# Kernel optimization log

Measured on AMD Instinct MI355X. Metric: run time of the kernel, lower is better.

Reference implementation:

```python
import jax, jax.numpy as jnp
import numpy as np

I_DIM, H_DIM, O_DIM = 4, 8, 1


def setup_inputs() -> dict:
    key = jax.random.key(0)
    ks = jax.random.split(key, 7)
    B, T = 8192, 512
    s_ih = 1.0 / np.sqrt(H_DIM)
    x = jax.random.normal(ks[0], (B, T, I_DIM), dtype=jnp.float32)
    # PyTorch LSTM params: gate order i, f, g, o stacked along first axis (4H)
    W_ih = jax.random.uniform(ks[1], (4 * H_DIM, I_DIM), jnp.float32, -s_ih, s_ih)
    W_hh = jax.random.uniform(ks[2], (4 * H_DIM, H_DIM), jnp.float32, -s_ih, s_ih)
    b_ih = jax.random.uniform(ks[3], (4 * H_DIM,), jnp.float32, -s_ih, s_ih)
    b_hh = jax.random.uniform(ks[4], (4 * H_DIM,), jnp.float32, -s_ih, s_ih)
    W_fc = jax.random.uniform(ks[5], (O_DIM, H_DIM), jnp.float32, -s_ih, s_ih)
    b_fc = jax.random.uniform(ks[6], (O_DIM,), jnp.float32, -s_ih, s_ih)
    return {"x": x, "W_ih": W_ih, "W_hh": W_hh, "b_ih": b_ih, "b_hh": b_hh,
            "W_fc": W_fc, "b_fc": b_fc}


def _lstm_last_hidden(x, W_ih, W_hh, b_ih, b_hh):
    B, T, _ = x.shape
    H = W_hh.shape[1]
    # Precompute input projections for all timesteps: [B, T, 4H] -> [T, B, 4H]
    xg = jnp.einsum('bti,gi->btg', x, W_ih) + b_ih + b_hh
    xg = jnp.transpose(xg, (1, 0, 2))
    h0 = jnp.zeros((B, H), x.dtype)
    c0 = jnp.zeros((B, H), x.dtype)

    def step(carry, g_t):
        h, c = carry
        gates = g_t + h @ W_hh.T  # [B, 4H]
        i, f, g, o = jnp.split(gates, 4, axis=-1)
        i = jax.nn.sigmoid(i)
        f = jax.nn.sigmoid(f)
        g = jnp.tanh(g)
        o = jax.nn.sigmoid(o)
        c = f * c + i * g
        h = o * jnp.tanh(c)
        return (h, c), None

    (h_last, _), _ = jax.lax.scan(step, (h0, c0), xg)
    return h_last  # equals out[:, -1, :]


def reference(x, W_ih, W_hh, b_ih, b_hh, W_fc, b_fc):
    h_last = _lstm_last_hidden(x, W_ih, W_hh, b_ih, b_hh)
    return h_last @ W_fc.T + b_fc  # [B, output_dim]
```

## Files before the change

kernel.cpp:

```cpp
#include <hip/hip_runtime.h>

#define T_STEPS 512
#define CHUNK   32
#define NCHUNK  (T_STEPS / CHUNK)
#define EPB     32
#define ROWF    132
#define BUFF    (EPB * ROWF)
#define LOG2E   1.4426950408889634f

typedef float v2f __attribute__((ext_vector_type(2)));

__device__ __forceinline__ v2f pk_fma_b(v2f w, float s, v2f c) {
    v2f sv; sv.x = s;
    v2f d;
    asm("v_pk_fma_f32 %0, %1, %2, %3 op_sel_hi:[1,0,1]"
        : "=v"(d) : "v"(w), "v"(sv), "v"(c));
    return d;
}
__device__ __forceinline__ void pk_fma_acc(v2f& a, v2f w, float s) {
    v2f sv; sv.x = s;
    asm("v_pk_fma_f32 %0, %1, %2, %0 op_sel_hi:[1,0,1]"
        : "+v"(a) : "v"(w), "v"(sv));
}
__device__ __forceinline__ v2f pk_mul_b(v2f w, float s) {
    v2f sv; sv.x = s;
    v2f d;
    asm("v_pk_mul_f32 %0, %1, %2 op_sel_hi:[1,0]"
        : "=v"(d) : "v"(w), "v"(sv));
    return d;
}
__device__ __forceinline__ v2f pk_add2(v2f a, v2f b) {
    v2f d;
    asm("v_pk_add_f32 %0, %1, %2" : "=v"(d) : "v"(a), "v"(b));
    return d;
}

template <int CTRL>
__device__ __forceinline__ float dppf(float v) {
    return __int_as_float(__builtin_amdgcn_update_dpp(
        0, __float_as_int(v), CTRL, 0xF, 0xF, true));
}

__global__ __launch_bounds__(256) void lstm_kernel(
    const float* __restrict__ x, const float* __restrict__ W_ih,
    const float* __restrict__ W_hh, const float* __restrict__ b_ih,
    const float* __restrict__ b_hh, const float* __restrict__ W_fc,
    const float* __restrict__ b_fc, float* __restrict__ out, int B)
{
    __shared__ float ldsx[2 * BUFF];

    const int tid = threadIdx.x;
    const int e   = tid >> 3;
    const int j   = tid & 7;

    const float nL  = -LOG2E;
    const float n2L = -2.0f * LOG2E;
    const float P2L =  2.0f * LOG2E;

    const int ri = j, rf = 8 + j, rg = 16 + j, ro = 24 + j;
    v2f wihIF[4], wihGO[4], whhIF[8], whhGO[8], biasIF, biasGO;
    #pragma unroll
    for (int k = 0; k < 4; ++k) {
        wihIF[k] = v2f{nL  * W_ih[ri * 4 + k], nL * W_ih[rf * 4 + k]};
        wihGO[k] = v2f{n2L * W_ih[rg * 4 + k], nL * W_ih[ro * 4 + k]};
    }
    #pragma unroll
    for (int s = 0; s < 8; ++s) {
        const int m = j ^ s;
        whhIF[s] = v2f{nL  * W_hh[ri * 8 + m], nL * W_hh[rf * 8 + m]};
        whhGO[s] = v2f{n2L * W_hh[rg * 8 + m], nL * W_hh[ro * 8 + m]};
    }
    biasIF = v2f{nL  * (b_ih[ri] + b_hh[ri]), nL * (b_ih[rf] + b_hh[rf])};
    biasGO = v2f{n2L * (b_ih[rg] + b_hh[rg]), nL * (b_ih[ro] + b_hh[ro])};

    const int st  = tid & 31;
    const int se0 = tid >> 5;
    const float* gp0 = x + (size_t)(blockIdx.x * EPB + se0) * (T_STEPS * 4) + st * 4;
    const int wl0 = se0 * ROWF + st * 4;

    float4 v0, v1, v2, v3;
    v0 = *(const float4*)(gp0);
    v1 = *(const float4*)(gp0 + 8 * 2048);
    v2 = *(const float4*)(gp0 + 16 * 2048);
    v3 = *(const float4*)(gp0 + 24 * 2048);
    *(float4*)&ldsx[wl0 + 0 * 8 * ROWF] = v0;
    *(float4*)&ldsx[wl0 + 1 * 8 * ROWF] = v1;
    *(float4*)&ldsx[wl0 + 2 * 8 * ROWF] = v2;
    *(float4*)&ldsx[wl0 + 3 * 8 * ROWF] = v3;
    v0 = *(const float4*)(gp0 + CHUNK * 4);
    v1 = *(const float4*)(gp0 + CHUNK * 4 + 8 * 2048);
    v2 = *(const float4*)(gp0 + CHUNK * 4 + 16 * 2048);
    v3 = *(const float4*)(gp0 + CHUNK * 4 + 24 * 2048);
    __syncthreads();

    float h = 0.0f, ct = 0.0f;

    for (int n = 0; n < NCHUNK; ++n) {
        const int wb = ((n + 1) & 1) * BUFF + wl0;
        *(float4*)&ldsx[wb + 0 * 8 * ROWF] = v0;
        *(float4*)&ldsx[wb + 1 * 8 * ROWF] = v1;
        *(float4*)&ldsx[wb + 2 * 8 * ROWF] = v2;
        *(float4*)&ldsx[wb + 3 * 8 * ROWF] = v3;
        const int t2 = ((n + 2) & (NCHUNK - 1)) * (CHUNK * 4);
        v0 = *(const float4*)(gp0 + t2);
        v1 = *(const float4*)(gp0 + t2 + 8 * 2048);
        v2 = *(const float4*)(gp0 + t2 + 16 * 2048);
        v3 = *(const float4*)(gp0 + t2 + 24 * 2048);

        const float* xr = &ldsx[(n & 1) * BUFF + e * ROWF];
        float4 xc = *(const float4*)(xr);
        #pragma unroll
        for (int t = 0; t < CHUNK; ++t) {
            const float4 xn = *(const float4*)(xr + (((t + 1) & (CHUNK - 1)) * 4));
            const float4 xt = xc;

            v2f xIF = pk_fma_b(wihIF[0], xt.x, biasIF);
            v2f xGO = pk_fma_b(wihGO[0], xt.x, biasGO);
            pk_fma_acc(xIF, wihIF[1], xt.y);  pk_fma_acc(xGO, wihGO[1], xt.y);
            pk_fma_acc(xIF, wihIF[2], xt.z);  pk_fma_acc(xGO, wihGO[2], xt.z);
            pk_fma_acc(xIF, wihIF[3], xt.w);  pk_fma_acc(xGO, wihGO[3], xt.w);

            const float s1 = dppf<0xB1>(h);
            const float s2 = dppf<0x4E>(h);
            const float s3 = dppf<0x1B>(h);
            const float s7 = dppf<0x141>(h);
            const float s4 = dppf<0x1B>(s7);
            const float s5 = dppf<0x4E>(s7);
            const float s6 = dppf<0xB1>(s7);

            v2f aIF = pk_fma_b(whhIF[0], h,  xIF);
            v2f bIF = pk_mul_b(whhIF[1], s1);
            v2f aGO = pk_fma_b(whhGO[0], h,  xGO);
            v2f bGO = pk_mul_b(whhGO[1], s1);
            pk_fma_acc(aIF, whhIF[2], s2);    pk_fma_acc(aGO, whhGO[2], s2);
            pk_fma_acc(bIF, whhIF[3], s3);    pk_fma_acc(bGO, whhGO[3], s3);
            pk_fma_acc(aIF, whhIF[4], s4);    pk_fma_acc(aGO, whhGO[4], s4);
            pk_fma_acc(bIF, whhIF[5], s5);    pk_fma_acc(bGO, whhGO[5], s5);
            pk_fma_acc(aIF, whhIF[6], s6);    pk_fma_acc(aGO, whhGO[6], s6);
            pk_fma_acc(bIF, whhIF[7], s7);    pk_fma_acc(bGO, whhGO[7], s7);
            const v2f gIF = pk_add2(aIF, bIF);
            const v2f gGO = pk_add2(aGO, bGO);

            const float eI = __builtin_amdgcn_exp2f(gIF.x);
            const float eF = __builtin_amdgcn_exp2f(gIF.y);
            const float eG = __builtin_amdgcn_exp2f(gGO.x);
            const float eO = __builtin_amdgcn_exp2f(gGO.y);

            const float R  = __builtin_amdgcn_rcpf((1.0f + eI) * (1.0f + eG));
            const float f_ = __builtin_amdgcn_rcpf(1.0f + eF);
            const float ign = fmaf(eG, P2L, n2L) * R;
            ct = fmaf(f_, ct, ign);
            const float eC = __builtin_amdgcn_exp2f(ct);
            const float RC = __builtin_amdgcn_rcpf((1.0f + eO) * (1.0f + eC));
            h = (1.0f - eC) * RC;

            xc = xn;
        }
        __syncthreads();
    }

    float pr = h * W_fc[j];
    pr += __shfl_xor(pr, 1);
    pr += __shfl_xor(pr, 2);
    pr += __shfl_xor(pr, 4);
    if (j == 0) out[blockIdx.x * EPB + e] = pr + b_fc[0];
}

extern "C" void kernel_launch(void* const* d_in, const int* in_sizes, int n_in,
                              void* d_out, int out_size, void* d_ws, size_t ws_size,
                              hipStream_t stream) {
    const float* x    = (const float*)d_in[0];
    const float* W_ih = (const float*)d_in[1];
    const float* W_hh = (const float*)d_in[2];
    const float* b_ih = (const float*)d_in[3];
    const float* b_hh = (const float*)d_in[4];
    const float* W_fc = (const float*)d_in[5];
    const float* b_fc = (const float*)d_in[6];
    float* out = (float*)d_out;

    const int B = in_sizes[0] / (T_STEPS * 4);
    const int block = 256;
    const int grid = (B * 8) / block;
    lstm_kernel<<<grid, block, 0, stream>>>(x, W_ih, W_hh, b_ih, b_hh, W_fc, b_fc, out, B);
}
```

Baseline: 172.9 us.

## Split each hidden unit's four LSTM gates across two lanes per element

Each batch element now gets 16 lanes instead of 8. Two lanes share one hidden unit: one lane computes the i/f gate pair and the other the g/o pair. The partial activations are swapped with a row-rotate DPP so both lanes can rebuild the cell and hidden state. The aim is to halve the serial per-step FMA chain in the latency-bound recurrence. The cost is twice as many threads, a doubled grid, duplicated cell/tanh work, extra DPP exchanges and selects, plus a launch_bounds hint of 2 blocks per SIMD unit that may limit registers.

```diff
diff --git a/kernel.cpp b/kernel.cpp
--- a/kernel.cpp
+++ b/kernel.cpp
@@ -3,7 +3,7 @@
 #define T_STEPS 512
 #define CHUNK   32
 #define NCHUNK  (T_STEPS / CHUNK)
-#define EPB     32
+#define EPB     16
 #define ROWF    132
 #define BUFF    (EPB * ROWF)
 #define LOG2E   1.4426950408889634f
@@ -41,7 +41,7 @@
         0, __float_as_int(v), CTRL, 0xF, 0xF, true));
 }
 
-__global__ __launch_bounds__(256) void lstm_kernel(
+__global__ __launch_bounds__(256, 2) void lstm_kernel(
     const float* __restrict__ x, const float* __restrict__ W_ih,
     const float* __restrict__ W_hh, const float* __restrict__ b_ih,
     const float* __restrict__ b_hh, const float* __restrict__ W_fc,
@@ -50,47 +50,45 @@
     __shared__ float ldsx[2 * BUFF];
 
     const int tid = threadIdx.x;
-    const int e   = tid >> 3;
-    const int j   = tid & 7;
+    const int e   = tid >> 4;
+    const int l   = tid & 15;
+    const int j   = l & 7;
+    const int p   = l >> 3;
 
     const float nL  = -LOG2E;
     const float n2L = -2.0f * LOG2E;
-    const float P2L =  2.0f * LOG2E;
 
-    const int ri = j, rf = 8 + j, rg = 16 + j, ro = 24 + j;
-    v2f wihIF[4], wihGO[4], whhIF[8], whhGO[8], biasIF, biasGO;
+    const int rowA = p ? (16 + j) : j;
+    const int rowB = p ? (24 + j) : (8 + j);
+    const float scA = p ? n2L : nL;
+    const float scB = nL;
+    const float cp = p ? 1.0f : n2L;
+    const float dp = p ? -1.0f : 0.0f;
+    const bool isP1 = (p != 0);
+
+    v2f wih[4], whh[8], bias;
     #pragma unroll
-    for (int k = 0; k < 4; ++k) {
-        wihIF[k] = v2f{nL  * W_ih[ri * 4 + k], nL * W_ih[rf * 4 + k]};
-        wihGO[k] = v2f{n2L * W_ih[rg * 4 + k], nL * W_ih[ro * 4 + k]};
-    }
+    for (int k = 0; k < 4; ++k)
+        wih[k] = v2f{scA * W_ih[rowA * 4 + k], scB * W_ih[rowB * 4 + k]};
     #pragma unroll
     for (int s = 0; s < 8; ++s) {
         const int m = j ^ s;
-        whhIF[s] = v2f{nL  * W_hh[ri * 8 + m], nL * W_hh[rf * 8 + m]};
-        whhGO[s] = v2f{n2L * W_hh[rg * 8 + m], nL * W_hh[ro * 8 + m]};
+        whh[s] = v2f{scA * W_hh[rowA * 8 + m], scB * W_hh[rowB * 8 + m]};
     }
-    biasIF = v2f{nL  * (b_ih[ri] + b_hh[ri]), nL * (b_ih[rf] + b_hh[rf])};
-    biasGO = v2f{n2L * (b_ih[rg] + b_hh[rg]), nL * (b_ih[ro] + b_hh[ro])};
+    bias = v2f{scA * (b_ih[rowA] + b_hh[rowA]), scB * (b_ih[rowB] + b_hh[rowB])};
 
     const int st  = tid & 31;
     const int se0 = tid >> 5;
     const float* gp0 = x + (size_t)(blockIdx.x * EPB + se0) * (T_STEPS * 4) + st * 4;
     const int wl0 = se0 * ROWF + st * 4;
 
-    float4 v0, v1, v2, v3;
+    float4 v0, v1;
     v0 = *(const float4*)(gp0);
     v1 = *(const float4*)(gp0 + 8 * 2048);
-    v2 = *(const float4*)(gp0 + 16 * 2048);
-    v3 = *(const float4*)(gp0 + 24 * 2048);
     *(float4*)&ldsx[wl0 + 0 * 8 * ROWF] = v0;
     *(float4*)&ldsx[wl0 + 1 * 8 * ROWF] = v1;
-    *(float4*)&ldsx[wl0 + 2 * 8 * ROWF] = v2;
-    *(float4*)&ldsx[wl0 + 3 * 8 * ROWF] = v3;
     v0 = *(const float4*)(gp0 + CHUNK * 4);
     v1 = *(const float4*)(gp0 + CHUNK * 4 + 8 * 2048);
-    v2 = *(const float4*)(gp0 + CHUNK * 4 + 16 * 2048);
-    v3 = *(const float4*)(gp0 + CHUNK * 4 + 24 * 2048);
     __syncthreads();
 
     float h = 0.0f, ct = 0.0f;
@@ -99,13 +97,9 @@
         const int wb = ((n + 1) & 1) * BUFF + wl0;
         *(float4*)&ldsx[wb + 0 * 8 * ROWF] = v0;
         *(float4*)&ldsx[wb + 1 * 8 * ROWF] = v1;
-        *(float4*)&ldsx[wb + 2 * 8 * ROWF] = v2;
-        *(float4*)&ldsx[wb + 3 * 8 * ROWF] = v3;
         const int t2 = ((n + 2) & (NCHUNK - 1)) * (CHUNK * 4);
         v0 = *(const float4*)(gp0 + t2);
         v1 = *(const float4*)(gp0 + t2 + 8 * 2048);
-        v2 = *(const float4*)(gp0 + t2 + 16 * 2048);
-        v3 = *(const float4*)(gp0 + t2 + 24 * 2048);
 
         const float* xr = &ldsx[(n & 1) * BUFF + e * ROWF];
         float4 xc = *(const float4*)(xr);
@@ -114,11 +108,10 @@
             const float4 xn = *(const float4*)(xr + (((t + 1) & (CHUNK - 1)) * 4));
             const float4 xt = xc;
 
-            v2f xIF = pk_fma_b(wihIF[0], xt.x, biasIF);
-            v2f xGO = pk_fma_b(wihGO[0], xt.x, biasGO);
-            pk_fma_acc(xIF, wihIF[1], xt.y);  pk_fma_acc(xGO, wihGO[1], xt.y);
-            pk_fma_acc(xIF, wihIF[2], xt.z);  pk_fma_acc(xGO, wihGO[2], xt.z);
-            pk_fma_acc(xIF, wihIF[3], xt.w);  pk_fma_acc(xGO, wihGO[3], xt.w);
+            v2f xp = pk_fma_b(wih[0], xt.x, bias);
+            pk_fma_acc(xp, wih[1], xt.y);
+            pk_fma_acc(xp, wih[2], xt.z);
+            pk_fma_acc(xp, wih[3], xt.w);
 
             const float s1 = dppf<0xB1>(h);
             const float s2 = dppf<0x4E>(h);
@@ -128,31 +121,38 @@
             const float s5 = dppf<0x4E>(s7);
             const float s6 = dppf<0xB1>(s7);
 
-            v2f aIF = pk_fma_b(whhIF[0], h,  xIF);
-            v2f bIF = pk_mul_b(whhIF[1], s1);
-            v2f aGO = pk_fma_b(whhGO[0], h,  xGO);
-            v2f bGO = pk_mul_b(whhGO[1], s1);
-            pk_fma_acc(aIF, whhIF[2], s2);    pk_fma_acc(aGO, whhGO[2], s2);
-            pk_fma_acc(bIF, whhIF[3], s3);    pk_fma_acc(bGO, whhGO[3], s3);
-            pk_fma_acc(aIF, whhIF[4], s4);    pk_fma_acc(aGO, whhGO[4], s4);
-            pk_fma_acc(bIF, whhIF[5], s5);    pk_fma_acc(bGO, whhGO[5], s5);
-            pk_fma_acc(aIF, whhIF[6], s6);    pk_fma_acc(aGO, whhGO[6], s6);
-            pk_fma_acc(bIF, whhIF[7], s7);    pk_fma_acc(bGO, whhGO[7], s7);
-            const v2f gIF = pk_add2(aIF, bIF);
-            const v2f gGO = pk_add2(aGO, bGO);
+            v2f a = pk_fma_b(whh[0], h, xp);
+            v2f b = pk_mul_b(whh[1], s1);
+            pk_fma_acc(a, whh[2], s2);
+            pk_fma_acc(b, whh[3], s3);
+            pk_fma_acc(a, whh[4], s4);
+            pk_fma_acc(b, whh[5], s5);
+            pk_fma_acc(a, whh[6], s6);
+            pk_fma_acc(b, whh[7], s7);
+            const v2f g2 = pk_add2(a, b);
 
-            const float eI = __builtin_amdgcn_exp2f(gIF.x);
-            const float eF = __builtin_amdgcn_exp2f(gIF.y);
-            const float eG = __builtin_amdgcn_exp2f(gGO.x);
-            const float eO = __builtin_amdgcn_exp2f(gGO.y);
+            const float eA = __builtin_amdgcn_exp2f(g2.x);
+            const float eB = __builtin_amdgcn_exp2f(g2.y);
+            const float q1 = 1.0f + eA;
+            const float q2 = 1.0f + eB;
+            const float R  = __builtin_amdgcn_rcpf(q1 * q2);
 
-            const float R  = __builtin_amdgcn_rcpf((1.0f + eI) * (1.0f + eG));
-            const float f_ = __builtin_amdgcn_rcpf(1.0f + eF);
-            const float ign = fmaf(eG, P2L, n2L) * R;
-            ct = fmaf(f_, ct, ign);
+            const float m_   = q2 * R;
+            const float tsc  = fmaf(eA, dp, cp);
+            const float actA = tsc * m_;
+            const float actB = q1 * R;
+
+            const float rA = dppf<0x128>(actA);
+            const float rB = dppf<0x128>(actB);
+
+            const float ig = actA * rA;
+            const float f_ = isP1 ? rB : actB;
+            const float o_ = isP1 ? actB : rB;
+
+            ct = fmaf(f_, ct, ig);
             const float eC = __builtin_amdgcn_exp2f(ct);
-            const float RC = __builtin_amdgcn_rcpf((1.0f + eO) * (1.0f + eC));
-            h = (1.0f - eC) * RC;
+            const float RC = __builtin_amdgcn_rcpf(1.0f + eC);
+            h = o_ * ((1.0f - eC) * RC);
 
             xc = xn;
         }
@@ -163,7 +163,7 @@
     pr += __shfl_xor(pr, 1);
     pr += __shfl_xor(pr, 2);
     pr += __shfl_xor(pr, 4);
-    if (j == 0) out[blockIdx.x * EPB + e] = pr + b_fc[0];
+    if (l == 0) out[blockIdx.x * EPB + e] = pr + b_fc[0];
 }
 
 extern "C" void kernel_launch(void* const* d_in, const int* in_sizes, int n_in,
@@ -180,6 +180,6 @@
 
     const int B = in_sizes[0] / (T_STEPS * 4);
     const int block = 256;
-    const int grid = (B * 8) / block;
+    const int grid = (B * 16) / block;
     lstm_kernel<<<grid, block, 0, stream>>>(x, W_ih, W_hh, b_ih, b_hh, W_fc, b_fc, out, B);
 }
```

New measurement: 193.8 us. 12.1% more time.
